# Optimization experiments

Measured on AMD Instinct MI355X. Metric: run time of the kernel, lower is better.

Reference implementation:

```python
import jax, jax.numpy as jnp
import numpy as np

N, E, D, H, C, L = 50000, 600000, 128, 128, 40, 2
NEG_SLOPE = 0.1


def setup_inputs() -> dict:
    key = jax.random.key(0)
    ks = jax.random.split(key, 12)

    def lin(k, din, dout):
        return (jax.random.normal(k, (din, dout), jnp.float32) / np.sqrt(din)).astype(jnp.float32)

    x = jax.random.normal(ks[0], (N, D), jnp.float32)
    edge_index = jax.random.randint(ks[1], (2, E), 0, N, dtype=jnp.int32)
    return {
        "x": x,
        "edge_index": edge_index,
        "enc_Wl": lin(ks[2], D, H),
        "enc_Wr": lin(ks[3], D, H),
        "enc_b": jnp.zeros((H,), jnp.float32),
        "lay_Wl": jnp.stack([lin(jax.random.fold_in(ks[4], i), H, H) for i in range(L)]),
        "lay_Wr": jnp.stack([lin(jax.random.fold_in(ks[5], i), H, H) for i in range(L)]),
        "lay_b": jnp.zeros((L, H), jnp.float32),
        "dec_Wl": lin(ks[6], H, C),
        "dec_Wr": lin(ks[7], H, C),
        "dec_b": jnp.zeros((C,), jnp.float32),
    }


def _sage(x, src, dst, inv_cnt, Wl, Wr, b):
    # mean-aggregate neighbor messages: gather x[src], scatter-sum to dst, divide by degree
    agg = jax.ops.segment_sum(x[src], dst, num_segments=N) * inv_cnt  # [N, d_in]
    return agg @ Wl + x @ Wr + b


def reference(x, edge_index, enc_Wl, enc_Wr, enc_b, lay_Wl, lay_Wr, lay_b, dec_Wl, dec_Wr, dec_b):
    src, dst = edge_index[0], edge_index[1]
    # in-degree per target node, clamped to 1 (PyG scatter-mean semantics: isolated nodes get 0)
    deg = jax.ops.segment_sum(jnp.ones((E,), jnp.float32), dst, num_segments=N)
    inv_cnt = (1.0 / jnp.maximum(deg, 1.0))[:, None]  # [N, 1]

    h = jax.nn.leaky_relu(_sage(x, src, dst, inv_cnt, enc_Wl, enc_Wr, enc_b), NEG_SLOPE)
    for i in range(L):
        h = jax.nn.leaky_relu(_sage(h, src, dst, inv_cnt, lay_Wl[i], lay_Wr[i], lay_b[i]), NEG_SLOPE)
    out = _sage(h, src, dst, inv_cnt, dec_Wl, dec_Wr, dec_b)
    return jax.nn.log_softmax(out, axis=1)
```

## Files before the change

kernel.cpp:

```cpp
#include <hip/hip_runtime.h>
#include <hip/hip_bf16.h>

#define NN 50000
#define EE 600000
#define HH 128
#define CC 40
#define NEG 0.1f
#define CAP 40

typedef __attribute__((ext_vector_type(8))) short bf16x8;
typedef __attribute__((ext_vector_type(4))) float f32x4;

__device__ __forceinline__ unsigned short f2bf(float f) {
    unsigned u = __float_as_uint(f);
    unsigned r = u + 0x7fffu + ((u >> 16) & 1u);
    return (unsigned short)(r >> 16);
}
__device__ __forceinline__ float bfhi(unsigned v) { return __uint_as_float(v & 0xFFFF0000u); }
__device__ __forceinline__ float bflo(unsigned v) { return __uint_as_float(v << 16); }

__global__ void k_build(const int* __restrict__ src, const int* __restrict__ dst,
                        int* __restrict__ counts, int* __restrict__ csr) {
    int e = blockIdx.x * blockDim.x + threadIdx.x;
    if (e < EE) {
        int d = dst[e];
        if ((unsigned)d < (unsigned)NN) {
            int sl = atomicAdd(&counts[d], 1);
            if (sl < CAP) csr[d * CAP + sl] = src[e];
        }
    }
}

__global__ void k_xcast(const float* __restrict__ x, unsigned* __restrict__ xb) {
    int t = blockIdx.x * 256 + threadIdx.x;
    if (t < NN * HH / 4) {
        float4 v = ((const float4*)x)[t];
        uint2 o;
        o.x = ((unsigned)f2bf(v.y) << 16) | f2bf(v.x);
        o.y = ((unsigned)f2bf(v.w) << 16) | f2bf(v.z);
        ((uint2*)xb)[t] = o;
    }
}

struct SwzArgs {
    const float* src[8];
    unsigned short* dst[8];
    int* counts;
};

template <int DOUT, int DOUTP>
__device__ __forceinline__ void swz_one(const float* __restrict__ W,
                                        unsigned short* __restrict__ dstf, int idx) {
    int k = idx / DOUTP, n = idx % DOUTP;
    unsigned short val = (n < DOUT) ? f2bf(W[k * DOUT + n]) : (unsigned short)0;
    int kt = k >> 5, kin = k & 31, nt = n >> 4, nin = n & 15;
    int lane = ((kin >> 3) << 4) | nin;
    int j = kin & 7;
    int NT = DOUTP >> 4;
    dstf[(((kt * NT + nt) * 64) + lane) * 8 + j] = val;
}

__global__ void k_swz_all(SwzArgs a) {
    int b = blockIdx.x;
    int tid = b * 256 + threadIdx.x;
    if (tid < NN) a.counts[tid] = 0;
    if (b < 384) {
        int which = b >> 6;
        int idx = (b & 63) * 256 + threadIdx.x;
        swz_one<HH, HH>(a.src[which], a.dst[which], idx);
    } else {
        int bb = b - 384;
        int which = 6 + bb / 24;
        int idx = (bb % 24) * 256 + threadIdx.x;
        swz_one<CC, 48>(a.src[which], a.dst[which], idx);
    }
}

__global__ __launch_bounds__(512) void k_layer(
    const unsigned short* __restrict__ hin,
    const int* __restrict__ counts, const int* __restrict__ csr,
    const unsigned short* __restrict__ B1f, const unsigned short* __restrict__ B2f,
    const float* __restrict__ bias, unsigned short* __restrict__ out) {
    __shared__ unsigned lds[16][72];
    int wid = threadIdx.x >> 6;
    int lane = threadIdx.x & 63;
    int m0 = blockIdx.x * 16;
    int g = lane & 7;
    int s = lane >> 3;
    const uint4* hw4 = (const uint4*)hin;

    int beg[2], cnt[2];
    float sc[2];
    int maxd = 0;
#pragma unroll
    for (int n = 0; n < 2; ++n) {
        int node = m0 + wid * 2 + n;
        int c = counts[node];
        c = c < CAP ? c : CAP;
        beg[n] = node * CAP;
        cnt[n] = c;
        sc[n] = 1.0f / (float)(c > 0 ? c : 1);
        maxd = maxd > c ? maxd : c;
    }
    int rounds = (maxd + 7) >> 3;

    for (int ph = 0; ph < 2; ++ph) {
        float acc[2][8];
#pragma unroll
        for (int n = 0; n < 2; ++n)
#pragma unroll
            for (int d = 0; d < 8; ++d) acc[n][d] = 0.f;

        uint4 v[2]; int ok[2];
        auto issue = [&](int r, uint4* vv, int* okk) {
#pragma unroll
            for (int n = 0; n < 2; ++n) {
                int idx = r * 8 + s;
                int o = idx < cnt[n];
                int row = csr[beg[n] + (o ? idx : 0)];
                vv[n] = hw4[(size_t)row * 16 + ph * 8 + g];
                okk[n] = o;
            }
        };
        if (rounds > 0) {
            issue(0, v, ok);
            for (int r = 0; r < rounds; ++r) {
                uint4 vn[2]; int okn[2];
                bool more = (r + 1 < rounds);
                if (more) issue(r + 1, vn, okn);
#pragma unroll
                for (int n = 0; n < 2; ++n) {
                    if (ok[n]) {
                        acc[n][0] += bflo(v[n].x); acc[n][1] += bfhi(v[n].x);
                        acc[n][2] += bflo(v[n].y); acc[n][3] += bfhi(v[n].y);
                        acc[n][4] += bflo(v[n].z); acc[n][5] += bfhi(v[n].z);
                        acc[n][6] += bflo(v[n].w); acc[n][7] += bfhi(v[n].w);
                    }
                }
                if (more) {
#pragma unroll
                    for (int n = 0; n < 2; ++n) { v[n] = vn[n]; ok[n] = okn[n]; }
                }
            }
        }
#pragma unroll
        for (int n = 0; n < 2; ++n) {
#pragma unroll
            for (int d = 0; d < 8; ++d) {
                float t = acc[n][d];
                t += __shfl_xor(t, 8, 64);
                t += __shfl_xor(t, 16, 64);
                t += __shfl_xor(t, 32, 64);
                acc[n][d] = t;
            }
            if (s == 0) {
                uint4 w4;
                w4.x = ((unsigned)f2bf(acc[n][1] * sc[n]) << 16) | f2bf(acc[n][0] * sc[n]);
                w4.y = ((unsigned)f2bf(acc[n][3] * sc[n]) << 16) | f2bf(acc[n][2] * sc[n]);
                w4.z = ((unsigned)f2bf(acc[n][5] * sc[n]) << 16) | f2bf(acc[n][4] * sc[n]);
                w4.w = ((unsigned)f2bf(acc[n][7] * sc[n]) << 16) | f2bf(acc[n][6] * sc[n]);
                *(uint4*)&lds[wid * 2 + n][ph * 32 + g * 4] = w4;
            }
        }
    }
    __syncthreads();

    int nin = lane & 15;
    int kq = lane >> 4;
    const unsigned* arow = &lds[nin][0];

    f32x4 acc1 = (f32x4){0.f, 0.f, 0.f, 0.f};

#pragma unroll
    for (int kt = 0; kt < 4; ++kt) {
        bf16x8 a1 = *(const bf16x8*)(arow + kt * 16 + kq * 4);
        bf16x8 a2 = *(const bf16x8*)(hin + (size_t)(m0 + nin) * HH + kt * 32 + kq * 8);
        bf16x8 b1 = *(const bf16x8*)(B1f + (((kt * 8 + wid) * 64) + lane) * 8);
        acc1 = __builtin_amdgcn_mfma_f32_16x16x32_bf16(a1, b1, acc1, 0, 0, 0);
        bf16x8 b2 = *(const bf16x8*)(B2f + (((kt * 8 + wid) * 64) + lane) * 8);
        acc1 = __builtin_amdgcn_mfma_f32_16x16x32_bf16(a2, b2, acc1, 0, 0, 0);
    }

    int col = wid * 16 + nin;
    float bv = bias[col];
#pragma unroll
    for (int r = 0; r < 4; ++r) {
        int m = m0 + kq * 4 + r;
        float v = acc1[r] + bv;
        v = fmaxf(v, NEG * v);
        out[(size_t)m * HH + col] = f2bf(v);
    }
}

__global__ __launch_bounds__(256) void k_pre(const unsigned short* __restrict__ h1,
                                             const unsigned short* __restrict__ Bf,
                                             unsigned short* __restrict__ t) {
    int wave = (blockIdx.x * 256 + threadIdx.x) >> 6;
    int lane = threadIdx.x & 63;
    int m0 = wave * 16;
    if (m0 >= NN) return;
    int nin = lane & 15, kq = lane >> 4;
    f32x4 acc[3];
#pragma unroll
    for (int j = 0; j < 3; ++j) acc[j] = (f32x4){0.f, 0.f, 0.f, 0.f};
#pragma unroll
    for (int kt = 0; kt < 4; ++kt) {
        bf16x8 a = *(const bf16x8*)(h1 + (size_t)(m0 + nin) * HH + kt * 32 + kq * 8);
#pragma unroll
        for (int j = 0; j < 3; ++j) {
            bf16x8 b = *(const bf16x8*)(Bf + (((kt * 3 + j) * 64) + lane) * 8);
            acc[j] = __builtin_amdgcn_mfma_f32_16x16x32_bf16(a, b, acc[j], 0, 0, 0);
        }
    }
#pragma unroll
    for (int j = 0; j < 3; ++j) {
        int col = j * 16 + nin;
#pragma unroll
        for (int r = 0; r < 4; ++r) {
            int m = m0 + kq * 4 + r;
            t[(size_t)m * 64 + col] = f2bf(acc[j][r]);
        }
    }
    int col2 = 48 + nin;
#pragma unroll
    for (int r = 0; r < 4; ++r) t[(size_t)(m0 + kq * 4 + r) * 64 + col2] = 0;
}

__global__ __launch_bounds__(512) void k_dec(
    const unsigned short* __restrict__ tbuf,
    const unsigned short* __restrict__ h1,
    const int* __restrict__ counts, const int* __restrict__ csr,
    const unsigned short* __restrict__ B2f, const float* __restrict__ bias,
    float* __restrict__ out) {
    __shared__ float aggT[16][52];
    int wid = threadIdx.x >> 6;
    int lane = threadIdx.x & 63;
    int m0 = blockIdx.x * 16;
    int g = lane & 7;
    int s = lane >> 3;
    const uint4* t4 = (const uint4*)tbuf;

    int beg[2], cnt[2];
    float sc[2];
    int maxd = 0;
#pragma unroll
    for (int n = 0; n < 2; ++n) {
        int node = m0 + wid * 2 + n;
        int c = counts[node];
        c = c < CAP ? c : CAP;
        beg[n] = node * CAP;
        cnt[n] = c;
        sc[n] = 1.0f / (float)(c > 0 ? c : 1);
        maxd = maxd > c ? maxd : c;
    }
    int rounds = (maxd + 7) >> 3;

    float acc[2][8];
#pragma unroll
    for (int n = 0; n < 2; ++n)
#pragma unroll
        for (int d = 0; d < 8; ++d) acc[n][d] = 0.f;

    uint4 v[2]; int ok[2];
    auto issue = [&](int r, uint4* vv, int* okk) {
#pragma unroll
        for (int n = 0; n < 2; ++n) {
            int idx = r * 8 + s;
            int o = idx < cnt[n];
            int row = csr[beg[n] + (o ? idx : 0)];
            vv[n] = t4[(size_t)row * 8 + g];
            okk[n] = o;
        }
    };
    if (rounds > 0) {
        issue(0, v, ok);
        for (int r = 0; r < rounds; ++r) {
            uint4 vn[2]; int okn[2];
            bool more = (r + 1 < rounds);
            if (more) issue(r + 1, vn, okn);
#pragma unroll
            for (int n = 0; n < 2; ++n) {
                if (ok[n]) {
                    acc[n][0] += bflo(v[n].x); acc[n][1] += bfhi(v[n].x);
                    acc[n][2] += bflo(v[n].y); acc[n][3] += bfhi(v[n].y);
                    acc[n][4] += bflo(v[n].z); acc[n][5] += bfhi(v[n].z);
                    acc[n][6] += bflo(v[n].w); acc[n][7] += bfhi(v[n].w);
                }
            }
            if (more) {
#pragma unroll
                for (int n = 0; n < 2; ++n) { v[n] = vn[n]; ok[n] = okn[n]; }
            }
        }
    }
#pragma unroll
    for (int n = 0; n < 2; ++n) {
#pragma unroll
        for (int d = 0; d < 8; ++d) {
            float t = acc[n][d];
            t += __shfl_xor(t, 8, 64);
            t += __shfl_xor(t, 16, 64);
            t += __shfl_xor(t, 32, 64);
            acc[n][d] = t;
        }
        if (s == 0 && g < 6) {
            float4 p0, p1;
            p0.x = acc[n][0] * sc[n]; p0.y = acc[n][1] * sc[n];
            p0.z = acc[n][2] * sc[n]; p0.w = acc[n][3] * sc[n];
            p1.x = acc[n][4] * sc[n]; p1.y = acc[n][5] * sc[n];
            p1.z = acc[n][6] * sc[n]; p1.w = acc[n][7] * sc[n];
            *(float4*)&aggT[wid * 2 + n][8 * g] = p0;
            *(float4*)&aggT[wid * 2 + n][8 * g + 4] = p1;
        }
    }
    __syncthreads();
    if (wid != 0) return;

    int nin = lane & 15, kq = lane >> 4;
    f32x4 acc2[3];
#pragma unroll
    for (int j = 0; j < 3; ++j) acc2[j] = (f32x4){0.f, 0.f, 0.f, 0.f};
#pragma unroll
    for (int kt = 0; kt < 4; ++kt) {
        bf16x8 a2 = *(const bf16x8*)(h1 + (size_t)(m0 + nin) * HH + kt * 32 + kq * 8);
#pragma unroll
        for (int j = 0; j < 3; ++j) {
            bf16x8 b2 = *(const bf16x8*)(B2f + (((kt * 3 + j) * 64) + lane) * 8);
            acc2[j] = __builtin_amdgcn_mfma_f32_16x16x32_bf16(a2, b2, acc2[j], 0, 0, 0);
        }
    }
    float bv[3];
#pragma unroll
    for (int t = 0; t < 3; ++t) {
        int col = t * 16 + nin;
        bv[t] = (col < CC) ? bias[col] : 0.f;
    }
#pragma unroll
    for (int r = 0; r < 4; ++r) {
        int m = m0 + kq * 4 + r;
        int ml = kq * 4 + r;
        float v[3];
        float mx = -1e30f;
#pragma unroll
        for (int t = 0; t < 3; ++t) {
            int col = t * 16 + nin;
            v[t] = acc2[t][r] + aggT[ml][col] + bv[t];
            if (col < CC) mx = fmaxf(mx, v[t]);
        }
        for (int off = 1; off < 16; off <<= 1) mx = fmaxf(mx, __shfl_xor(mx, off, 64));
        float sm = 0.f;
#pragma unroll
        for (int t = 0; t < 3; ++t) {
            int col = t * 16 + nin;
            if (col < CC) sm += expf(v[t] - mx);
        }
        for (int off = 1; off < 16; off <<= 1) sm += __shfl_xor(sm, off, 64);
        float lse = mx + logf(sm);
#pragma unroll
        for (int t = 0; t < 3; ++t) {
            int col = t * 16 + nin;
            if (col < CC) out[(size_t)m * CC + col] = v[t] - lse;
        }
    }
}

extern "C" void kernel_launch(void* const* d_in, const int* in_sizes, int n_in,
                              void* d_out, int out_size, void* d_ws, size_t ws_size,
                              hipStream_t stream) {
    const float* x      = (const float*)d_in[0];
    const int*   ei     = (const int*)d_in[1];
    const float* enc_Wl = (const float*)d_in[2];
    const float* enc_Wr = (const float*)d_in[3];
    const float* enc_b  = (const float*)d_in[4];
    const float* lay_Wl = (const float*)d_in[5];
    const float* lay_Wr = (const float*)d_in[6];
    const float* lay_b  = (const float*)d_in[7];
    const float* dec_Wl = (const float*)d_in[8];
    const float* dec_Wr = (const float*)d_in[9];
    const float* dec_b  = (const float*)d_in[10];
    float* out = (float*)d_out;

    const int* src = ei;
    const int* dst = ei + EE;

    char* p = (char*)d_ws;
    auto carve = [&](size_t bytes) {
        char* r = p;
        p += (bytes + 255) & ~(size_t)255;
        return r;
    };
    int*            counts = (int*)carve(NN * 4);
    int*            csr    = (int*)carve((size_t)NN * CAP * 4);
    unsigned short* h1     = (unsigned short*)carve((size_t)NN * HH * 2);
    unsigned short* h2     = (unsigned short*)carve((size_t)NN * HH * 2);
    unsigned short* wf[8];
    for (int i = 0; i < 6; ++i) wf[i] = (unsigned short*)carve(HH * HH * 2);
    wf[6] = (unsigned short*)carve(HH * 48 * 2);
    wf[7] = (unsigned short*)carve(HH * 48 * 2);

    {
        SwzArgs a;
        a.src[0] = enc_Wl; a.src[1] = enc_Wr;
        a.src[2] = lay_Wl; a.src[3] = lay_Wr;
        a.src[4] = lay_Wl + HH * HH; a.src[5] = lay_Wr + HH * HH;
        a.src[6] = dec_Wl; a.src[7] = dec_Wr;
        for (int i = 0; i < 8; ++i) a.dst[i] = wf[i];
        a.counts = counts;
        k_swz_all<<<432, 256, 0, stream>>>(a);
    }

    k_build<<<(EE + 255) / 256, 256, 0, stream>>>(src, dst, counts, csr);

    k_xcast<<<(NN * HH / 4 + 255) / 256, 256, 0, stream>>>(x, (unsigned*)h2);

    const int FB = NN / 16;
    k_layer<<<FB, 512, 0, stream>>>(h2, counts, csr, wf[0], wf[1], enc_b,      h1);
    k_layer<<<FB, 512, 0, stream>>>(h1, counts, csr, wf[2], wf[3], lay_b,      h2);
    k_layer<<<FB, 512, 0, stream>>>(h2, counts, csr, wf[4], wf[5], lay_b + HH, h1);

    k_pre<<<(NN / 16 + 3) / 4, 256, 0, stream>>>(h1, wf[6], h2);
    k_dec<<<FB, 512, 0, stream>>>(h2, h1, counts, csr, wf[7], dec_b, out);
}
```

Measured before the change: 303.0 us.

## Fuse decoder pre-projection into last layer, merge prep kernels, shrink gather rows

Merges the x-to-bf16 cast into the weight-swizzle prep kernel, which removes one launch. Also fuses the decoder's h@Wl projection into the final hidden layer: the layer output tile is staged in LDS and three waves run MFMAs against the decoder weights, so h1 no longer has to be re-read by a separate k_pre kernel. The projected buffer is now 48 columns wide instead of padded to 64, which cuts the bytes k_dec gathers per neighbor. In exchange the last layer does extra work behind a block-wide sync, and lanes 6 and 7 of each 8-lane group now load duplicate chunks.

```diff
diff --git a/kernel.cpp b/kernel.cpp
--- a/kernel.cpp
+++ b/kernel.cpp
@@ -31,21 +31,12 @@
     }
 }
 
-__global__ void k_xcast(const float* __restrict__ x, unsigned* __restrict__ xb) {
-    int t = blockIdx.x * 256 + threadIdx.x;
-    if (t < NN * HH / 4) {
-        float4 v = ((const float4*)x)[t];
-        uint2 o;
-        o.x = ((unsigned)f2bf(v.y) << 16) | f2bf(v.x);
-        o.y = ((unsigned)f2bf(v.w) << 16) | f2bf(v.z);
-        ((uint2*)xb)[t] = o;
-    }
-}
-
-struct SwzArgs {
-    const float* src[8];
-    unsigned short* dst[8];
+struct PrepArgs {
+    const float* wsrc[8];
+    unsigned short* wdst[8];
     int* counts;
+    const float* x;
+    unsigned* xb;
 };
 
 template <int DOUT, int DOUTP>
@@ -60,27 +51,38 @@
     dstf[(((kt * NT + nt) * 64) + lane) * 8 + j] = val;
 }
 
-__global__ void k_swz_all(SwzArgs a) {
+__global__ void k_prep(PrepArgs a) {
     int b = blockIdx.x;
-    int tid = b * 256 + threadIdx.x;
-    if (tid < NN) a.counts[tid] = 0;
     if (b < 384) {
+        int tid = b * 256 + threadIdx.x;
+        if (tid < NN) a.counts[tid] = 0;
         int which = b >> 6;
         int idx = (b & 63) * 256 + threadIdx.x;
-        swz_one<HH, HH>(a.src[which], a.dst[which], idx);
-    } else {
+        swz_one<HH, HH>(a.wsrc[which], a.wdst[which], idx);
+    } else if (b < 432) {
         int bb = b - 384;
         int which = 6 + bb / 24;
         int idx = (bb % 24) * 256 + threadIdx.x;
-        swz_one<CC, 48>(a.src[which], a.dst[which], idx);
-    }
-}
-
+        swz_one<CC, 48>(a.wsrc[which], a.wdst[which], idx);
+    } else {
+        int t = (b - 432) * 256 + threadIdx.x;
+        if (t < NN * HH / 4) {
+            float4 v = ((const float4*)a.x)[t];
+            uint2 o;
+            o.x = ((unsigned)f2bf(v.y) << 16) | f2bf(v.x);
+            o.y = ((unsigned)f2bf(v.w) << 16) | f2bf(v.z);
+            ((uint2*)a.xb)[t] = o;
+        }
+    }
+}
+
+template <int MODE>
 __global__ __launch_bounds__(512) void k_layer(
     const unsigned short* __restrict__ hin,
     const int* __restrict__ counts, const int* __restrict__ csr,
     const unsigned short* __restrict__ B1f, const unsigned short* __restrict__ B2f,
-    const float* __restrict__ bias, unsigned short* __restrict__ out) {
+    const float* __restrict__ bias, unsigned short* __restrict__ out,
+    const unsigned short* __restrict__ Tf, unsigned short* __restrict__ tOut) {
     __shared__ unsigned lds[16][72];
     int wid = threadIdx.x >> 6;
     int lane = threadIdx.x & 63;
@@ -183,47 +185,37 @@
 
     int col = wid * 16 + nin;
     float bv = bias[col];
+    unsigned short hv[4];
 #pragma unroll
     for (int r = 0; r < 4; ++r) {
         int m = m0 + kq * 4 + r;
         float v = acc1[r] + bv;
         v = fmaxf(v, NEG * v);
-        out[(size_t)m * HH + col] = f2bf(v);
-    }
-}
-
-__global__ __launch_bounds__(256) void k_pre(const unsigned short* __restrict__ h1,
-                                             const unsigned short* __restrict__ Bf,
-                                             unsigned short* __restrict__ t) {
-    int wave = (blockIdx.x * 256 + threadIdx.x) >> 6;
-    int lane = threadIdx.x & 63;
-    int m0 = wave * 16;
-    if (m0 >= NN) return;
-    int nin = lane & 15, kq = lane >> 4;
-    f32x4 acc[3];
-#pragma unroll
-    for (int j = 0; j < 3; ++j) acc[j] = (f32x4){0.f, 0.f, 0.f, 0.f};
-#pragma unroll
-    for (int kt = 0; kt < 4; ++kt) {
-        bf16x8 a = *(const bf16x8*)(h1 + (size_t)(m0 + nin) * HH + kt * 32 + kq * 8);
-#pragma unroll
-        for (int j = 0; j < 3; ++j) {
-            bf16x8 b = *(const bf16x8*)(Bf + (((kt * 3 + j) * 64) + lane) * 8);
-            acc[j] = __builtin_amdgcn_mfma_f32_16x16x32_bf16(a, b, acc[j], 0, 0, 0);
-        }
-    }
-#pragma unroll
-    for (int j = 0; j < 3; ++j) {
-        int col = j * 16 + nin;
-#pragma unroll
-        for (int r = 0; r < 4; ++r) {
-            int m = m0 + kq * 4 + r;
-            t[(size_t)m * 64 + col] = f2bf(acc[j][r]);
-        }
-    }
-    int col2 = 48 + nin;
-#pragma unroll
-    for (int r = 0; r < 4; ++r) t[(size_t)(m0 + kq * 4 + r) * 64 + col2] = 0;
+        hv[r] = f2bf(v);
+        out[(size_t)m * HH + col] = hv[r];
+    }
+
+    if (MODE == 1) {
+        __syncthreads();
+        unsigned short* lsh = (unsigned short*)&lds[0][0];
+#pragma unroll
+        for (int r = 0; r < 4; ++r) lsh[(kq * 4 + r) * 144 + col] = hv[r];
+        __syncthreads();
+        if (wid < 3) {
+            f32x4 at = (f32x4){0.f, 0.f, 0.f, 0.f};
+#pragma unroll
+            for (int kt = 0; kt < 4; ++kt) {
+                bf16x8 a = *(const bf16x8*)&lsh[nin * 144 + kt * 32 + kq * 8];
+                bf16x8 b = *(const bf16x8*)(Tf + (((kt * 3 + wid) * 64) + lane) * 8);
+                at = __builtin_amdgcn_mfma_f32_16x16x32_bf16(a, b, at, 0, 0, 0);
+            }
+#pragma unroll
+            for (int r = 0; r < 4; ++r) {
+                int m = m0 + kq * 4 + r;
+                tOut[(size_t)m * 48 + wid * 16 + nin] = f2bf(at[r]);
+            }
+        }
+    }
 }
 
 __global__ __launch_bounds__(512) void k_dec(
@@ -237,6 +229,7 @@
     int lane = threadIdx.x & 63;
     int m0 = blockIdx.x * 16;
     int g = lane & 7;
+    int g6 = g < 6 ? g : g - 6;
     int s = lane >> 3;
     const uint4* t4 = (const uint4*)tbuf;
 
@@ -268,7 +261,7 @@
             int idx = r * 8 + s;
             int o = idx < cnt[n];
             int row = csr[beg[n] + (o ? idx : 0)];
-            vv[n] = t4[(size_t)row * 8 + g];
+            vv[n] = t4[(size_t)row * 6 + g6];
             okk[n] = o;
         }
     };
@@ -393,31 +386,31 @@
     int*            csr    = (int*)carve((size_t)NN * CAP * 4);
     unsigned short* h1     = (unsigned short*)carve((size_t)NN * HH * 2);
     unsigned short* h2     = (unsigned short*)carve((size_t)NN * HH * 2);
+    unsigned short* tbuf   = (unsigned short*)carve((size_t)NN * 48 * 2 + 256);
     unsigned short* wf[8];
     for (int i = 0; i < 6; ++i) wf[i] = (unsigned short*)carve(HH * HH * 2);
     wf[6] = (unsigned short*)carve(HH * 48 * 2);
     wf[7] = (unsigned short*)carve(HH * 48 * 2);
 
     {
-        SwzArgs a;
-        a.src[0] = enc_Wl; a.src[1] = enc_Wr;
-        a.src[2] = lay_Wl; a.src[3] = lay_Wr;
-        a.src[4] = lay_Wl + HH * HH; a.src[5] = lay_Wr + HH * HH;
-        a.src[6] = dec_Wl; a.src[7] = dec_Wr;
-        for (int i = 0; i < 8; ++i) a.dst[i] = wf[i];
+        PrepArgs a;
+        a.wsrc[0] = enc_Wl; a.wsrc[1] = enc_Wr;
+        a.wsrc[2] = lay_Wl; a.wsrc[3] = lay_Wr;
+        a.wsrc[4] = lay_Wl + HH * HH; a.wsrc[5] = lay_Wr + HH * HH;
+        a.wsrc[6] = dec_Wl; a.wsrc[7] = dec_Wr;
+        for (int i = 0; i < 8; ++i) a.wdst[i] = wf[i];
         a.counts = counts;
-        k_swz_all<<<432, 256, 0, stream>>>(a);
+        a.x = x;
+        a.xb = (unsigned*)h2;
+        k_prep<<<432 + (NN * HH / 4 + 255) / 256, 256, 0, stream>>>(a);
     }
 
     k_build<<<(EE + 255) / 256, 256, 0, stream>>>(src, dst, counts, csr);
 
-    k_xcast<<<(NN * HH / 4 + 255) / 256, 256, 0, stream>>>(x, (unsigned*)h2);
-
     const int FB = NN / 16;
-    k_layer<<<FB, 512, 0, stream>>>(h2, counts, csr, wf[0], wf[1], enc_b,      h1);
-    k_layer<<<FB, 512, 0, stream>>>(h1, counts, csr, wf[2], wf[3], lay_b,      h2);
-    k_layer<<<FB, 512, 0, stream>>>(h2, counts, csr, wf[4], wf[5], lay_b + HH, h1);
-
-    k_pre<<<(NN / 16 + 3) / 4, 256, 0, stream>>>(h1, wf[6], h2);
-    k_dec<<<FB, 512, 0, stream>>>(h2, h1, counts, csr, wf[7], dec_b, out);
-}
+    k_layer<0><<<FB, 512, 0, stream>>>(h2, counts, csr, wf[0], wf[1], enc_b,      h1, nullptr, nullptr);
+    k_layer<0><<<FB, 512, 0, stream>>>(h1, counts, csr, wf[2], wf[3], lay_b,      h2, nullptr, nullptr);
+    k_layer<1><<<FB, 512, 0, stream>>>(h2, counts, csr, wf[4], wf[5], lay_b + HH, h1, wf[6], tbuf);
+
+    k_dec<<<FB, 512, 0, stream>>>(tbuf, h1, counts, csr, wf[7], dec_b, out);
+}
```

Result: faster. 294.3 us (-2.9%).
